# Kernel tuning notes

Measured on AMD Instinct MI355X. Metric: run time of the kernel, lower is better.

Reference implementation:

```python
import jax, jax.numpy as jnp
import numpy as np

EPS_NORM = 1e-12  # F.normalize eps
LN_EPS = 1e-5


def _ln(x, g, b):
    mu = x.mean(-1, keepdims=True)
    var = ((x - mu) ** 2).mean(-1, keepdims=True)
    return (x - mu) / jnp.sqrt(var + LN_EPS) * g + b


def _gate(x, w1, b1, g, b, w2, b2):
    # Linear -> LayerNorm(32) -> SiLU -> Linear -> Sigmoid, squeeze(-1)
    t = _ln(x @ w1 + b1, g, b)
    t = jax.nn.silu(t)
    return jax.nn.sigmoid(t @ w2 + b2)[..., 0]


def setup_inputs() -> dict:
    key = jax.random.key(0)
    B, N, D, dH, S, HID = 4, 4096, 1024, 256, 256, 32
    ks = jax.random.split(key, 24)
    sc_d = 0.5 * (6.0 / (D + dH)) ** 0.5  # xavier gain=0.5 approx
    sc_h = 0.5 * (6.0 / (D + HID)) ** 0.5
    inp = {
        "h": jax.random.normal(ks[0], (B, N, D), jnp.float32),
        # encoder complex projection (stored as (in,out))
        "Wr": jax.random.uniform(ks[1], (D, dH), jnp.float32, -sc_d, sc_d),
        "br": jnp.zeros((dH,), jnp.float32),
        "Wi": jax.random.uniform(ks[2], (D, dH), jnp.float32, -sc_d, sc_d),
        "bi": jnp.zeros((dH,), jnp.float32),
        # uncertainty net
        "uw1": jax.random.uniform(ks[3], (D, HID), jnp.float32, -sc_h, sc_h),
        "ub1": jnp.zeros((HID,), jnp.float32),
        "ug": jnp.ones((HID,), jnp.float32),
        "ubeta": jnp.zeros((HID,), jnp.float32),
        "uw2": jax.random.uniform(ks[4], (HID, 1), jnp.float32, -0.2, 0.2),
        "ub2": jnp.zeros((1,), jnp.float32),
        # decoherence gamma net
        "gw1": jax.random.uniform(ks[5], (D, HID), jnp.float32, -sc_h, sc_h),
        "gb1": jnp.zeros((HID,), jnp.float32),
        "gg": jnp.ones((HID,), jnp.float32),
        "gbeta": jnp.zeros((HID,), jnp.float32),
        "gw2": jax.random.uniform(ks[6], (HID, 1), jnp.float32, -0.2, 0.2),
        "gb2": jnp.zeros((1,), jnp.float32),
        # memory attention params
        "m_real": jax.random.normal(ks[7], (S, dH), jnp.float32) / dH ** 0.5,
        "m_imag": jax.random.normal(ks[8], (S, dH), jnp.float32) / dH ** 0.5,
        "values": jax.random.normal(ks[9], (S, D), jnp.float32) * 0.02,
        "ow": jax.random.uniform(ks[10], (D, D), jnp.float32, -0.5 * (3.0 / D) ** 0.5, 0.5 * (3.0 / D) ** 0.5),
        "ob": jnp.zeros((D,), jnp.float32),
        # norms
        "n1g": jnp.ones((D,), jnp.float32),
        "n1b": jnp.zeros((D,), jnp.float32),
        "n2g": jnp.ones((D,), jnp.float32),
        "n2b": jnp.zeros((D,), jnp.float32),
        # FFN
        "fw1": jax.random.normal(ks[11], (D, 4 * D), jnp.float32) * (2.0 / (5 * D)) ** 0.5,
        "fb1": jnp.zeros((4 * D,), jnp.float32),
        "fw2": jax.random.normal(ks[12], (4 * D, D), jnp.float32) * (2.0 / (5 * D)) ** 0.5,
        "fb2": jnp.zeros((D,), jnp.float32),
    }
    return inp


def reference(h, Wr, br, Wi, bi,
              uw1, ub1, ug, ubeta, uw2, ub2,
              gw1, gb1, gg, gbeta, gw2, gb2,
              m_real, m_imag, values, ow, ob,
              n1g, n1b, n2g, n2b, fw1, fb1, fw2, fb2):
    dH = m_real.shape[-1]
    # --- QuantumStateEncoder: psi = normalize(complex(Wr h, Wi h)), p in [0,0.95]
    pr = h @ Wr + br                       # (B,N,dH) real part
    pi = h @ Wi + bi                       # (B,N,dH) imag part
    nrm = jnp.maximum(jnp.sqrt(jnp.sum(pr * pr + pi * pi, -1, keepdims=True)), EPS_NORM)
    pr, pi = pr / nrm, pi / nrm
    p_init = _gate(h, uw1, ub1, ug, ubeta, uw2, ub2) * 0.95   # (B,N)
    # --- ContextualDecoherenceLayer: ctx = mean over N (identical per token)
    ctx = h.mean(axis=1)                   # (B,D)
    gamma = _gate(ctx, gw1, gb1, gg, gbeta, gw2, gb2)          # (B,)
    p = p_init * (1.0 - gamma[:, None])    # (B,N)
    # --- ExternalQuantumMemoryAttention
    mnrm = jnp.maximum(jnp.sqrt(jnp.sum(m_real * m_real + m_imag * m_imag, -1, keepdims=True)), EPS_NORM)
    Mr, Mi = m_real / mnrm, m_imag / mnrm  # (S,dH)
    # <psi|m> = sum conj(psi)*m ; |.|^2 is re^2+im^2
    re = jnp.einsum('bnd,sd->bns', pr, Mr) + jnp.einsum('bnd,sd->bns', pi, Mi)
    im = jnp.einsum('bnd,sd->bns', pr, Mi) - jnp.einsum('bnd,sd->bns', pi, Mr)
    overlap = re * re + im * im            # (B,N,S)
    raw = (1.0 - p)[..., None] * overlap + (p / dH)[..., None]
    attn = raw / (raw.sum(-1, keepdims=True) + 1e-8)
    attn_out = jnp.einsum('bns,sd->bnd', attn, values) @ ow + ob
    # --- residual + LN + FFN (dropout = eval identity)
    h1 = _ln(h + attn_out, n1g, n1b)
    ff = jax.nn.gelu(h1 @ fw1 + fb1, approximate=False) @ fw2 + fb2
    return _ln(h1 + ff, n2g, n2b)
```

## Files before the change

### kernel.cpp

```cpp
#include <hip/hip_runtime.h>
#include <math.h>


#define B_ 4
#define N_ 4096
#define D_ 1024
#define DH_ 256
#define S_ 256
#define HID_ 32
#define M_ (B_ * N_)

typedef unsigned short u16;
typedef unsigned int u32;
typedef __attribute__((ext_vector_type(8))) short bfrag;
typedef __attribute__((ext_vector_type(4))) float ffrag;

__device__ __forceinline__ float b2f(u16 u) {
    return __uint_as_float(((unsigned)u) << 16);
}
__device__ __forceinline__ u16 f2b(float f) {
    unsigned u = __float_as_uint(f);
    return (u16)((u + 0x7FFFu + ((u >> 16) & 1u)) >> 16);
}
__device__ __forceinline__ float fast_erf(float x) {
    float ax = fabsf(x);
    float t = __builtin_amdgcn_rcpf(fmaf(0.3275911f, ax, 1.f));
    float p = t * fmaf(t, fmaf(t, fmaf(t, fmaf(t, 1.061405429f, -1.453152027f),
                                       1.421413741f), -0.284496736f),
                       0.254829592f);
    float e = __expf(-ax * ax);
    float y = fmaf(-p, e, 1.f);
    return copysignf(y, x);
}
__device__ __forceinline__ float gelu_fast(float x) {
    return 0.5f * x * (1.0f + fast_erf(x * 0.70710678118654752440f));
}
__device__ __forceinline__ float ldf(const void* p, size_t i, bool bf) {
    return bf ? b2f(((const u16*)p)[i]) : ((const float*)p)[i];
}
__device__ __forceinline__ bool detect_bf(const void* n1g) {
    return *(const unsigned*)n1g == 0x3F803F80u;
}
__device__ __forceinline__ void gload16(const void* g, void* lds) {
    __builtin_amdgcn_global_load_lds(
        (const __attribute__((address_space(1))) u32*)g,
        (__attribute__((address_space(3))) u32*)lds, 16, 0, 0);
}

__global__ void zero_kernel(float* __restrict__ p, int n) {
    int i = blockIdx.x * 256 + threadIdx.x;
    if (i < n) p[i] = 0.f;
}

__global__ __launch_bounds__(256)
void h2b_kernel(const void* __restrict__ h, u16* __restrict__ hB,
                const void* __restrict__ n1g) {
    const bool bf = detect_bf(n1g);
    const size_t i = ((size_t)blockIdx.x * 256 + threadIdx.x) * 8;
    if (bf) {
        *(uint4*)(hB + i) = *(const uint4*)((const u16*)h + i);
    } else {
        const float* hf = (const float*)h;
        float4 x = *(const float4*)(hf + i);
        float4 y = *(const float4*)(hf + i + 4);
        union { u16 u[8]; uint4 v; } pk;
        pk.u[0] = f2b(x.x); pk.u[1] = f2b(x.y);
        pk.u[2] = f2b(x.z); pk.u[3] = f2b(x.w);
        pk.u[4] = f2b(y.x); pk.u[5] = f2b(y.y);
        pk.u[6] = f2b(y.z); pk.u[7] = f2b(y.w);
        *(uint4*)(hB + i) = pk.v;
    }
}

__global__ void pack_bias_kernel(const void* __restrict__ br,
                                 const void* __restrict__ bi,
                                 void* __restrict__ brbi,
                                 const void* __restrict__ n1g) {
    const bool bf = detect_bf(n1g);
    const int t = threadIdx.x;
    if (bf) {
        ((u16*)brbi)[t]       = ((const u16*)br)[t];
        ((u16*)brbi)[256 + t] = ((const u16*)bi)[t];
    } else {
        ((float*)brbi)[t]       = ((const float*)br)[t];
        ((float*)brbi)[256 + t] = ((const float*)bi)[t];
    }
}

__global__ __launch_bounds__(256)
void transpose_w_kernel(const void* __restrict__ W, u16* __restrict__ WT,
                        int K, int N, const void* __restrict__ n1g) {
    const bool bf = detect_bf(n1g);
    __shared__ u16 t[64][65];
    const int n0 = blockIdx.x * 64, k0 = blockIdx.y * 64;
    const int a = threadIdx.x & 63, b = threadIdx.x >> 6;
#pragma unroll
    for (int r = 0; r < 16; ++r) {
        int k = b * 16 + r;
        t[k][a] = f2b(ldf(W, (size_t)(k0 + k) * N + n0 + a, bf));
    }
    __syncthreads();
#pragma unroll
    for (int r = 0; r < 16; ++r) {
        int n = b * 16 + r;
        WT[(size_t)(n0 + n) * K + k0 + a] = t[a][n];
    }
}

__global__ __launch_bounds__(256)
void ctx_sum_kernel(const u16* __restrict__ hB, float* __restrict__ ctx) {
    const int chunks = N_ / 128;
    const int b = blockIdx.x / chunks;
    const int ch = blockIdx.x % chunks;
    const int tid = threadIdx.x;
    const size_t base = ((size_t)b * N_ + (size_t)ch * 128) * D_;
    float a[4] = {0.f, 0.f, 0.f, 0.f};
    for (int r = 0; r < 128; ++r)
#pragma unroll
        for (int q = 0; q < 4; ++q)
            a[q] += b2f(hB[base + (size_t)r * D_ + q * 256 + tid]);
#pragma unroll
    for (int q = 0; q < 4; ++q)
        atomicAdd(&ctx[b * D_ + q * 256 + tid], a[q]);
}

__global__ __launch_bounds__(128)
void gamma_gate_kernel(const float* __restrict__ ctx,
                       const void* __restrict__ w1, const void* __restrict__ b1,
                       const void* __restrict__ g, const void* __restrict__ beta,
                       const void* __restrict__ w2, const void* __restrict__ b2,
                       float* __restrict__ out, const void* __restrict__ n1g) {
    const bool bf = detect_bf(n1g);
    const int row = blockIdx.x;
    const int tid = threadIdx.x;
    const int col = tid & 31;
    const int chunk = tid >> 5;
    const float xscale = 1.f / (float)N_;

    float acc = 0.f;
    for (int k = chunk * 256; k < chunk * 256 + 256; ++k)
        acc += ctx[(size_t)row * D_ + k] * xscale * ldf(w1, (size_t)k * HID_ + col, bf);

    __shared__ float part[4][HID_];
    __shared__ float s[HID_];
    __shared__ float mu_s, rstd_s;
    part[chunk][col] = acc;
    __syncthreads();
    if (tid < HID_)
        s[tid] = part[0][tid] + part[1][tid] + part[2][tid] + part[3][tid]
               + ldf(b1, tid, bf);
    __syncthreads();
    if (tid == 0) {
        float m = 0.f;
        for (int i = 0; i < HID_; ++i) m += s[i];
        m /= (float)HID_;
        float var = 0.f;
        for (int i = 0; i < HID_; ++i) { float dd = s[i] - m; var += dd * dd; }
        var /= (float)HID_;
        mu_s = m;
        rstd_s = rsqrtf(var + 1e-5f);
    }
    __syncthreads();
    if (tid < HID_) {
        float v = (s[tid] - mu_s) * rstd_s * ldf(g, tid, bf) + ldf(beta, tid, bf);
        v = v / (1.f + expf(-v));
        s[tid] = v * ldf(w2, tid, bf);
    }
    __syncthreads();
    if (tid == 0) {
        float z = 0.f;
        for (int i = 0; i < HID_; ++i) z += s[i];
        z += ldf(b2, 0, bf);
        out[row] = 1.f / (1.f + expf(-z));
    }
}

__global__ __launch_bounds__(128)
void p_gate_kernel(const u16* __restrict__ hB,
                   const void* __restrict__ w1, const void* __restrict__ b1,
                   const void* __restrict__ g, const void* __restrict__ beta,
                   const void* __restrict__ w2, const void* __restrict__ b2,
                   float* __restrict__ out, const void* __restrict__ n1g) {
    const bool bf = detect_bf(n1g);
    const int row = blockIdx.x;
    const int tid = threadIdx.x;
    const int col = tid & 31;
    const int chunk = tid >> 5;

    float acc = 0.f;
    for (int k = chunk * 256; k < chunk * 256 + 256; ++k)
        acc += b2f(hB[(size_t)row * D_ + k]) * ldf(w1, (size_t)k * HID_ + col, bf);

    __shared__ float part[4][HID_];
    __shared__ float s[HID_];
    __shared__ float mu_s, rstd_s;
    part[chunk][col] = acc;
    __syncthreads();
    if (tid < HID_)
        s[tid] = part[0][tid] + part[1][tid] + part[2][tid] + part[3][tid]
               + ldf(b1, tid, bf);
    __syncthreads();
    if (tid == 0) {
        float m = 0.f;
        for (int i = 0; i < HID_; ++i) m += s[i];
        m /= (float)HID_;
        float var = 0.f;
        for (int i = 0; i < HID_; ++i) { float dd = s[i] - m; var += dd * dd; }
        var /= (float)HID_;
        mu_s = m;
        rstd_s = rsqrtf(var + 1e-5f);
    }
    __syncthreads();
    if (tid < HID_) {
        float v = (s[tid] - mu_s) * rstd_s * ldf(g, tid, bf) + ldf(beta, tid, bf);
        v = v / (1.f + expf(-v));
        s[tid] = v * ldf(w2, tid, bf);
    }
    __syncthreads();
    if (tid == 0) {
        float z = 0.f;
        for (int i = 0; i < HID_; ++i) z += s[i];
        z += ldf(b2, 0, bf);
        out[row] = 0.95f / (1.f + expf(-z));
    }
}

__global__ __launch_bounds__(256)
void norm_m_kernel(const void* __restrict__ m_real, const void* __restrict__ m_imag,
                   u16* __restrict__ bcatT, const void* __restrict__ n1g) {
    const bool bf = detect_bf(n1g);
    const int s = blockIdx.x;
    const int d = threadIdx.x;
    float mr = ldf(m_real, (size_t)s * DH_ + d, bf);
    float mi = ldf(m_imag, (size_t)s * DH_ + d, bf);
    float v = mr * mr + mi * mi;
#pragma unroll
    for (int off = 32; off; off >>= 1) v += __shfl_down(v, off, 64);
    __shared__ float red[4];
    if ((d & 63) == 0) red[d >> 6] = v;
    __syncthreads();
    float tot = red[0] + red[1] + red[2] + red[3];
    float inv = 1.f / fmaxf(sqrtf(tot), 1e-12f);
    float nr = mr * inv, ni = mi * inv;
    bcatT[(size_t)s * 512 + d]               = f2b(nr);
    bcatT[(size_t)s * 512 + 256 + d]         = f2b(ni);
    bcatT[(size_t)(256 + s) * 512 + d]       = f2b(ni);
    bcatT[(size_t)(256 + s) * 512 + 256 + d] = f2b(-nr);
}

__global__ __launch_bounds__(256)
void gemm_mfma(const u16* __restrict__ A, const u16* __restrict__ WT,
               const void* __restrict__ bias, void* __restrict__ out,
               int N, int kseg, int lda, int ldw, int ldo,
               int act, int fo32, int accum, const void* __restrict__ n1g) {
    const bool bf = detect_bf(n1g);
    __shared__ short As[128 * 64];
    __shared__ short Bs[128 * 64];
    const int tid = threadIdx.x;

    const int nwg = gridDim.x * gridDim.y;
    const int flat = blockIdx.y * gridDim.x + blockIdx.x;
    const int xcd = flat & 7, idx = flat >> 3;
    const int qq = nwg >> 3, rr = nwg & 7;
    const int nf = (xcd < rr ? xcd * (qq + 1) : rr * (qq + 1) + (xcd - rr) * qq) + idx;
    const int c0 = (nf % gridDim.x) * 128;
    const int r0 = (nf / gridDim.x) * 128;

    const int kz = blockIdx.z * kseg;
    const int lane = tid & 63, wave = tid >> 6;
    const int wm = wave & 1, wn = wave >> 1;
    const int quad = lane >> 4, l15 = lane & 15;
    const int l8 = lane >> 3;
    const int lc = (lane & 7) ^ l8;
    const int sx = l15 & 7;

    ffrag acc[4][4];
#pragma unroll
    for (int i = 0; i < 4; ++i)
#pragma unroll
        for (int j = 0; j < 4; ++j)
            acc[i][j] = (ffrag){0.f, 0.f, 0.f, 0.f};

    for (int k0 = kz; k0 < kz + kseg; k0 += 64) {
        __syncthreads();
#pragma unroll
        for (int i = 0; i < 4; ++i) {
            int rb = wave * 32 + i * 8;
            gload16(A + (size_t)(r0 + rb + l8) * lda + k0 + lc * 8,
                    &As[rb * 64]);
        }
#pragma unroll
        for (int i = 0; i < 4; ++i) {
            int rb = wave * 32 + i * 8;
            gload16(WT + (size_t)(c0 + rb + l8) * ldw + k0 + lc * 8,
                    &Bs[rb * 64]);
        }
        __syncthreads();

#pragma unroll
        for (int ks = 0; ks < 2; ++ks) {
            bfrag a[4], b[4];
#pragma unroll
            for (int i = 0; i < 4; ++i) {
                int row = wm * 64 + i * 16 + l15;
                a[i] = *(const bfrag*)&As[row * 64 + (((ks * 4 + quad) ^ sx) * 8)];
            }
#pragma unroll
            for (int j = 0; j < 4; ++j) {
                int row = wn * 64 + j * 16 + l15;
                b[j] = *(const bfrag*)&Bs[row * 64 + (((ks * 4 + quad) ^ sx) * 8)];
            }
#pragma unroll
            for (int i = 0; i < 4; ++i)
#pragma unroll
                for (int j = 0; j < 4; ++j)
                    acc[i][j] = __builtin_amdgcn_mfma_f32_16x16x32_bf16(
                        a[i], b[j], acc[i][j], 0, 0, 0);
        }
    }

    const bool addb = bias && (blockIdx.z == 0);
    float bv[4];
#pragma unroll
    for (int j = 0; j < 4; ++j)
        bv[j] = addb ? ldf(bias, c0 + wn * 64 + j * 16 + l15, bf) : 0.f;
#pragma unroll
    for (int i = 0; i < 4; ++i)
#pragma unroll
        for (int r = 0; r < 4; ++r) {
            int row_g = r0 + wm * 64 + i * 16 + quad * 4 + r;
#pragma unroll
            for (int j = 0; j < 4; ++j) {
                int col_g = c0 + wn * 64 + j * 16 + l15;
                float v = acc[i][j][r] + bv[j];
                if (act) v = gelu_fast(v);
                if (accum)
                    atomicAdd(&((float*)out)[(size_t)row_g * ldo + col_g], v);
                else if (fo32)
                    ((float*)out)[(size_t)row_g * ldo + col_g] = v;
                else
                    ((u16*)out)[(size_t)row_g * ldo + col_g] = f2b(v);
            }
        }
}

#define TPW 8
__global__ __launch_bounds__(256)
void attn_weights_kernel(const u16* __restrict__ psi,
                         const float* __restrict__ reim,
                         const float* __restrict__ p_init,
                         const float* __restrict__ gamma,
                         u16* __restrict__ a2) {
    const int token0 = blockIdx.x * TPW;
    const int tid = threadIdx.x;
    __shared__ float red[4];

    for (int tt = 0; tt < TPW; ++tt) {
        const size_t t = (size_t)(token0 + tt);
        float x0 = b2f(psi[t * 512 + tid]);
        float x1 = b2f(psi[t * 512 + 256 + tid]);
        float v = x0 * x0 + x1 * x1;
#pragma unroll
        for (int off = 32; off; off >>= 1) v += __shfl_down(v, off, 64);
        if ((tid & 63) == 0) red[tid >> 6] = v;
        __syncthreads();
        float inv = 1.f / fmaxf(red[0] + red[1] + red[2] + red[3], 1e-24f);

        float p = p_init[t] * (1.f - gamma[t / N_]);
        float re = reim[t * 512 + tid];
        float im = reim[t * 512 + 256 + tid];
        float raw = (1.f - p) * (re * re + im * im) * inv + p * (1.f / (float)DH_);

        float w = raw;
#pragma unroll
        for (int off = 32; off; off >>= 1) w += __shfl_down(w, off, 64);
        __syncthreads();
        if ((tid & 63) == 0) red[tid >> 6] = w;
        __syncthreads();
        float denom = red[0] + red[1] + red[2] + red[3];
        a2[t * 256 + tid] = f2b(raw / (denom + 1e-8f));
        __syncthreads();
    }
}

__global__ __launch_bounds__(256)
void copy_rows_kernel(const u16* __restrict__ src, u16* __restrict__ dst) {
    const int row = blockIdx.x;
    const int tid = threadIdx.x;
#pragma unroll
    for (int q = 0; q < 4; ++q)
        dst[(size_t)row * D_ + q * 256 + tid] = src[(size_t)row * D_ + q * 256 + tid];
}

__global__ __launch_bounds__(256)
void ln_add_kernel(const void* __restrict__ x, int xmode, size_t xrow0,
                   const void* __restrict__ y, int ymode,
                   const void* __restrict__ g, const void* __restrict__ b,
                   u16* __restrict__ outB, float* __restrict__ outF,
                   const void* __restrict__ n1g) {
    const bool bfin = detect_bf(n1g);
    const bool bfx = (xmode == 1) ? true : bfin;
    const int row = blockIdx.x;
    const int tid = threadIdx.x;
    __shared__ float red[4];

    float v[4];
#pragma unroll
    for (int q = 0; q < 4; ++q) {
        int d = q * 256 + tid;
        float yv = ymode ? ((const float*)y)[(size_t)row * D_ + d]
                         : b2f(((const u16*)y)[(size_t)row * D_ + d]);
        v[q] = ldf(x, (xrow0 + row) * (size_t)D_ + d, bfx) + yv;
    }

    float s = v[0] + v[1] + v[2] + v[3];
#pragma unroll
    for (int off = 32; off; off >>= 1) s += __shfl_down(s, off, 64);
    if ((tid & 63) == 0) red[tid >> 6] = s;
    __syncthreads();
    float mu = (red[0] + red[1] + red[2] + red[3]) * (1.f / (float)D_);
    __syncthreads();

    float q2 = 0.f;
#pragma unroll
    for (int j = 0; j < 4; ++j) { float dd = v[j] - mu; q2 += dd * dd; }
#pragma unroll
    for (int off = 32; off; off >>= 1) q2 += __shfl_down(q2, off, 64);
    if ((tid & 63) == 0) red[tid >> 6] = q2;
    __syncthreads();
    float var = (red[0] + red[1] + red[2] + red[3]) * (1.f / (float)D_);
    float rstd = rsqrtf(var + 1e-5f);

#pragma unroll
    for (int q = 0; q < 4; ++q) {
        int d = q * 256 + tid;
        float o = (v[q] - mu) * rstd * ldf(g, d, bfin) + ldf(b, d, bfin);
        if (outF) outF[(size_t)row * D_ + d] = o;
        else      outB[(size_t)row * D_ + d] = f2b(o);
    }
}

extern "C" void kernel_launch(void* const* d_in, const int* in_sizes, int n_in,
                              void* d_out, int out_size, void* d_ws, size_t ws_size,
                              hipStream_t stream) {
    const void* h      = d_in[0];
    const void* Wr     = d_in[1];
    const void* br     = d_in[2];
    const void* Wi     = d_in[3];
    const void* bi     = d_in[4];
    const void* uw1    = d_in[5];
    const void* ub1    = d_in[6];
    const void* ug     = d_in[7];
    const void* ubeta  = d_in[8];
    const void* uw2    = d_in[9];
    const void* ub2    = d_in[10];
    const void* gw1    = d_in[11];
    const void* gb1    = d_in[12];
    const void* gg     = d_in[13];
    const void* gbeta  = d_in[14];
    const void* gw2    = d_in[15];
    const void* gb2    = d_in[16];
    const void* m_real = d_in[17];
    const void* m_imag = d_in[18];
    const void* values = d_in[19];
    const void* ow     = d_in[20];
    const void* ob     = d_in[21];
    const void* n1g    = d_in[22];
    const void* n1b    = d_in[23];
    const void* n2g    = d_in[24];
    const void* n2b    = d_in[25];
    const void* fw1    = d_in[26];
    const void* fb1    = d_in[27];
    const void* fw2    = d_in[28];
    const void* fb2    = d_in[29];

    char*  ws      = (char*)d_ws;
    float* ctx     = (float*)(ws);
    float* gammap  = (float*)(ws + 16384);
    float* p_init  = (float*)(ws + 16448);
    void*  brbi    = (void*)(ws + 81984);
    u16*   BCatT   = (u16*)(ws + 84032);
    u16*   WrT     = (u16*)(ws + 608320);
    u16*   WiT     = (u16*)(ws + 1132608);
    u16*   valuesT = (u16*)(ws + 1656896);
    u16*   owT     = (u16*)(ws + 2181184);
    u16*   fw1T    = (u16*)(ws + 4278336);
    u16*   fw2T    = (u16*)(ws + 12666944);
    const size_t tbase = 21055552;

    int CH = 16384;
    while (CH > 128 && tbase + (size_t)CH * 12288 > ws_size) CH >>= 1;
    u16*   t_buf = (u16*)(ws + tbase);
    float* pf    = (float*)(t_buf + (size_t)CH * 4096);

    float* outF   = (float*)d_out;
    u16*   Psi    = (u16*)d_out;
    u16*   A2     = Psi + (size_t)M_ * 512;
    u16*   X2     = (u16*)d_out + (size_t)M_ * D_;
    u16*   hB     = X2;
    float* REIMf  = (float*)X2;

    h2b_kernel<<<M_ * D_ / 2048, 256, 0, stream>>>(h, hB, n1g);

    transpose_w_kernel<<<dim3(DH_ / 64, D_ / 64), 256, 0, stream>>>(Wr, WrT, D_, DH_, n1g);
    transpose_w_kernel<<<dim3(DH_ / 64, D_ / 64), 256, 0, stream>>>(Wi, WiT, D_, DH_, n1g);
    transpose_w_kernel<<<dim3(D_ / 64, S_ / 64), 256, 0, stream>>>(values, valuesT, S_, D_, n1g);
    transpose_w_kernel<<<dim3(D_ / 64, D_ / 64), 256, 0, stream>>>(ow, owT, D_, D_, n1g);
    transpose_w_kernel<<<dim3(4 * D_ / 64, D_ / 64), 256, 0, stream>>>(fw1, fw1T, D_, 4 * D_, n1g);
    transpose_w_kernel<<<dim3(D_ / 64, 4 * D_ / 64), 256, 0, stream>>>(fw2, fw2T, 4 * D_, D_, n1g);
    pack_bias_kernel<<<1, 256, 0, stream>>>(br, bi, brbi, n1g);

    zero_kernel<<<16, 256, 0, stream>>>(ctx, B_ * D_);
    ctx_sum_kernel<<<B_ * (N_ / 128), 256, 0, stream>>>(hB, ctx);
    gamma_gate_kernel<<<B_, 128, 0, stream>>>(ctx, gw1, gb1, gg, gbeta,
                                              gw2, gb2, gammap, n1g);

    norm_m_kernel<<<S_, 256, 0, stream>>>(m_real, m_imag, BCatT, n1g);

    gemm_mfma<<<dim3(512 / 128, M_ / 128), 256, 0, stream>>>(
        hB, WrT, brbi, Psi, 512, D_, D_, D_, 512, 0, 0, 0, n1g);

    p_gate_kernel<<<M_, 128, 0, stream>>>(hB, uw1, ub1, ug, ubeta,
                                          uw2, ub2, p_init, n1g);

    gemm_mfma<<<dim3(512 / 128, M_ / 128), 256, 0, stream>>>(
        Psi, BCatT, nullptr, REIMf, 512, 512, 512, 512, 512, 0, 1, 0, n1g);

    attn_weights_kernel<<<M_ / TPW, 256, 0, stream>>>(Psi, REIMf, p_init,
                                                      gammap, A2);

    gemm_mfma<<<dim3(D_ / 128, M_ / 128), 256, 0, stream>>>(
        A2, valuesT, nullptr, X2, D_, S_, S_, S_, D_, 0, 0, 0, n1g);

    const int gy = CH / 128;
    auto pick_split = [&](int gx) {
        int ks = 1;
        while (gx * gy * ks < 512 && ks < 8) ks <<= 1;
        return ks;
    };

    {
        const int ks = pick_split(D_ / 128);
        for (int c = 0; c < M_ / CH; ++c) {
            const size_t off = (size_t)c * CH * D_;
            if (ks > 1)
                zero_kernel<<<(CH * D_ + 255) / 256, 256, 0, stream>>>(pf, CH * D_);
            gemm_mfma<<<dim3(D_ / 128, gy, ks), 256, 0, stream>>>(
                X2 + off, owT, ob, pf, D_, D_ / ks, D_, D_, D_, 0, 1, ks > 1, n1g);
            ln_add_kernel<<<CH, 256, 0, stream>>>(h, 0, (size_t)c * CH, pf, 1,
                                                  n1g, n1b, X2 + off, nullptr, n1g);
        }
    }

    {
        const int ks2 = pick_split(D_ / 128);
        for (int c = 0; c < M_ / CH; ++c) {
            const size_t off = (size_t)c * CH * D_;
            gemm_mfma<<<dim3(4 * D_ / 128, gy), 256, 0, stream>>>(
                X2 + off, fw1T, fb1, t_buf, 4 * D_, D_, D_, D_, 4 * D_, 1, 0, 0, n1g);
            if (ks2 > 1)
                zero_kernel<<<(CH * D_ + 255) / 256, 256, 0, stream>>>(pf, CH * D_);
            gemm_mfma<<<dim3(D_ / 128, gy, ks2), 256, 0, stream>>>(
                t_buf, fw2T, fb2, pf, D_, 4 * D_ / ks2, 4 * D_, 4 * D_, D_, 0, 1, ks2 > 1, n1g);
            copy_rows_kernel<<<CH, 256, 0, stream>>>(X2 + off, t_buf);
            ln_add_kernel<<<CH, 256, 0, stream>>>(t_buf, 1, 0, pf, 1,
                                                  n2g, n2b, nullptr, outF + off, n1g);
        }
    }
}
```

Before: 1.068 ms.

## Add 256x256 double-buffered MFMA GEMM and drop split-K atomics for large GEMMs

Adds a new 512-thread GEMM kernel with 256x256 output tiles, double-buffered LDS staging overlapped via vmcnt waits, and raised wave priority during the MFMA phase. It is used for the values, output-projection and both FFN GEMMs. The split-K path with atomicAdd and its zeroing kernels is removed. Larger tiles raise data reuse and cut global traffic. The cost is higher register and LDS use (128 KB LDS per block), which lowers occupancy, and fewer workgroups when the chunk size is small.

Result: faster. 1.013 ms (-5.2%).

```diff
diff --git a/kernel.cpp b/kernel.cpp
--- a/kernel.cpp
+++ b/kernel.cpp
@@ -251,8 +251,8 @@
 __global__ __launch_bounds__(256)
 void gemm_mfma(const u16* __restrict__ A, const u16* __restrict__ WT,
                const void* __restrict__ bias, void* __restrict__ out,
-               int N, int kseg, int lda, int ldw, int ldo,
-               int act, int fo32, int accum, const void* __restrict__ n1g) {
+               int kseg, int lda, int ldw, int ldo,
+               int act, int fo32, const void* __restrict__ n1g) {
     const bool bf = detect_bf(n1g);
     __shared__ short As[128 * 64];
     __shared__ short Bs[128 * 64];
@@ -266,7 +266,6 @@
     const int c0 = (nf % gridDim.x) * 128;
     const int r0 = (nf / gridDim.x) * 128;
 
-    const int kz = blockIdx.z * kseg;
     const int lane = tid & 63, wave = tid >> 6;
     const int wm = wave & 1, wn = wave >> 1;
     const int quad = lane >> 4, l15 = lane & 15;
@@ -281,19 +280,17 @@
         for (int j = 0; j < 4; ++j)
             acc[i][j] = (ffrag){0.f, 0.f, 0.f, 0.f};
 
-    for (int k0 = kz; k0 < kz + kseg; k0 += 64) {
+    for (int k0 = 0; k0 < kseg; k0 += 64) {
         __syncthreads();
 #pragma unroll
         for (int i = 0; i < 4; ++i) {
             int rb = wave * 32 + i * 8;
-            gload16(A + (size_t)(r0 + rb + l8) * lda + k0 + lc * 8,
-                    &As[rb * 64]);
+            gload16(A + (size_t)(r0 + rb + l8) * lda + k0 + lc * 8, &As[rb * 64]);
         }
 #pragma unroll
         for (int i = 0; i < 4; ++i) {
             int rb = wave * 32 + i * 8;
-            gload16(WT + (size_t)(c0 + rb + l8) * ldw + k0 + lc * 8,
-                    &Bs[rb * 64]);
+            gload16(WT + (size_t)(c0 + rb + l8) * ldw + k0 + lc * 8, &Bs[rb * 64]);
         }
         __syncthreads();
 
@@ -319,11 +316,10 @@
         }
     }
 
-    const bool addb = bias && (blockIdx.z == 0);
     float bv[4];
 #pragma unroll
     for (int j = 0; j < 4; ++j)
-        bv[j] = addb ? ldf(bias, c0 + wn * 64 + j * 16 + l15, bf) : 0.f;
+        bv[j] = bias ? ldf(bias, c0 + wn * 64 + j * 16 + l15, bf) : 0.f;
 #pragma unroll
     for (int i = 0; i < 4; ++i)
 #pragma unroll
@@ -334,12 +330,112 @@
                 int col_g = c0 + wn * 64 + j * 16 + l15;
                 float v = acc[i][j][r] + bv[j];
                 if (act) v = gelu_fast(v);
-                if (accum)
-                    atomicAdd(&((float*)out)[(size_t)row_g * ldo + col_g], v);
-                else if (fo32)
-                    ((float*)out)[(size_t)row_g * ldo + col_g] = v;
-                else
-                    ((u16*)out)[(size_t)row_g * ldo + col_g] = f2b(v);
+                if (fo32) ((float*)out)[(size_t)row_g * ldo + col_g] = v;
+                else      ((u16*)out)[(size_t)row_g * ldo + col_g] = f2b(v);
+            }
+        }
+}
+
+__global__ __launch_bounds__(512, 2)
+void gemm_mfma2(const u16* __restrict__ A, const u16* __restrict__ WT,
+                const void* __restrict__ bias, void* __restrict__ out,
+                int K, int lda, int ldw, int ldo,
+                int act, int fo32, const void* __restrict__ n1g) {
+    const bool bf = detect_bf(n1g);
+    __shared__ short As[2][256 * 64];
+    __shared__ short Bs[2][256 * 64];
+    const int tid = threadIdx.x;
+
+    const int nwg = gridDim.x * gridDim.y;
+    const int flat = blockIdx.y * gridDim.x + blockIdx.x;
+    const int xcd = flat & 7, idx = flat >> 3;
+    const int qq = nwg >> 3, rr = nwg & 7;
+    const int nf = (xcd < rr ? xcd * (qq + 1) : rr * (qq + 1) + (xcd - rr) * qq) + idx;
+    const int c0 = (nf % gridDim.x) * 256;
+    const int r0 = (nf / gridDim.x) * 256;
+
+    const int lane = tid & 63, wave = tid >> 6;
+    const int wm = wave & 1, wn = wave >> 1;
+    const int quad = lane >> 4, l15 = lane & 15;
+    const int l8 = lane >> 3;
+    const int lc = (lane & 7) ^ l8;
+    const int sx = l15 & 7;
+
+    ffrag acc[8][4];
+#pragma unroll
+    for (int i = 0; i < 8; ++i)
+#pragma unroll
+        for (int j = 0; j < 4; ++j)
+            acc[i][j] = (ffrag){0.f, 0.f, 0.f, 0.f};
+
+    auto STAGE = [&](int buf, int k0) {
+#pragma unroll
+        for (int r = 0; r < 4; ++r) {
+            int rb = r * 64 + wave * 8;
+            gload16(A + (size_t)(r0 + rb + l8) * lda + k0 + lc * 8,
+                    &As[buf][rb * 64]);
+        }
+#pragma unroll
+        for (int r = 0; r < 4; ++r) {
+            int rb = r * 64 + wave * 8;
+            gload16(WT + (size_t)(c0 + rb + l8) * ldw + k0 + lc * 8,
+                    &Bs[buf][rb * 64]);
+        }
+    };
+
+    const int nt = K >> 6;
+    STAGE(0, 0);
+    int cur = 0;
+    for (int t = 0; t < nt; ++t) {
+        if (t + 1 < nt) {
+            STAGE(cur ^ 1, (t + 1) << 6);
+            asm volatile("s_waitcnt vmcnt(8)" ::: "memory");
+        } else {
+            asm volatile("s_waitcnt vmcnt(0)" ::: "memory");
+        }
+        __builtin_amdgcn_s_barrier();
+        __builtin_amdgcn_sched_barrier(0);
+        __builtin_amdgcn_s_setprio(1);
+#pragma unroll
+        for (int ks = 0; ks < 2; ++ks) {
+            bfrag a[8], b[4];
+#pragma unroll
+            for (int j = 0; j < 4; ++j) {
+                int row = wn * 64 + j * 16 + l15;
+                b[j] = *(const bfrag*)&Bs[cur][row * 64 + (((ks * 4 + quad) ^ sx) * 8)];
+            }
+#pragma unroll
+            for (int i = 0; i < 8; ++i) {
+                int row = wm * 128 + i * 16 + l15;
+                a[i] = *(const bfrag*)&As[cur][row * 64 + (((ks * 4 + quad) ^ sx) * 8)];
+#pragma unroll
+                for (int j = 0; j < 4; ++j)
+                    acc[i][j] = __builtin_amdgcn_mfma_f32_16x16x32_bf16(
+                        a[i], b[j], acc[i][j], 0, 0, 0);
+            }
+        }
+        __builtin_amdgcn_s_setprio(0);
+        __builtin_amdgcn_sched_barrier(0);
+        __builtin_amdgcn_s_barrier();
+        cur ^= 1;
+    }
+
+    float bv[4];
+#pragma unroll
+    for (int j = 0; j < 4; ++j)
+        bv[j] = bias ? ldf(bias, c0 + wn * 64 + j * 16 + l15, bf) : 0.f;
+#pragma unroll
+    for (int i = 0; i < 8; ++i)
+#pragma unroll
+        for (int r = 0; r < 4; ++r) {
+            int row_g = r0 + wm * 128 + i * 16 + quad * 4 + r;
+#pragma unroll
+            for (int j = 0; j < 4; ++j) {
+                int col_g = c0 + wn * 64 + j * 16 + l15;
+                float v = acc[i][j][r] + bv[j];
+                if (act) v = gelu_fast(v);
+                if (fo32) ((float*)out)[(size_t)row_g * ldo + col_g] = v;
+                else      ((u16*)out)[(size_t)row_g * ldo + col_g] = f2b(v);
             }
         }
 }
@@ -489,7 +585,7 @@
     const size_t tbase = 21055552;
 
     int CH = 16384;
-    while (CH > 128 && tbase + (size_t)CH * 12288 > ws_size) CH >>= 1;
+    while (CH > 256 && tbase + (size_t)CH * 12288 > ws_size) CH >>= 1;
     u16*   t_buf = (u16*)(ws + tbase);
     float* pf    = (float*)(t_buf + (size_t)CH * 4096);
 
@@ -518,53 +614,36 @@
     norm_m_kernel<<<S_, 256, 0, stream>>>(m_real, m_imag, BCatT, n1g);
 
     gemm_mfma<<<dim3(512 / 128, M_ / 128), 256, 0, stream>>>(
-        hB, WrT, brbi, Psi, 512, D_, D_, D_, 512, 0, 0, 0, n1g);
+        hB, WrT, brbi, Psi, D_, D_, D_, 512, 0, 0, n1g);
 
     p_gate_kernel<<<M_, 128, 0, stream>>>(hB, uw1, ub1, ug, ubeta,
                                           uw2, ub2, p_init, n1g);
 
     gemm_mfma<<<dim3(512 / 128, M_ / 128), 256, 0, stream>>>(
-        Psi, BCatT, nullptr, REIMf, 512, 512, 512, 512, 512, 0, 1, 0, n1g);
+        Psi, BCatT, nullptr, REIMf, 512, 512, 512, 512, 0, 1, n1g);
 
     attn_weights_kernel<<<M_ / TPW, 256, 0, stream>>>(Psi, REIMf, p_init,
                                                       gammap, A2);
 
-    gemm_mfma<<<dim3(D_ / 128, M_ / 128), 256, 0, stream>>>(
-        A2, valuesT, nullptr, X2, D_, S_, S_, S_, D_, 0, 0, 0, n1g);
-
-    const int gy = CH / 128;
-    auto pick_split = [&](int gx) {
-        int ks = 1;
-        while (gx * gy * ks < 512 && ks < 8) ks <<= 1;
-        return ks;
-    };
-
-    {
-        const int ks = pick_split(D_ / 128);
-        for (int c = 0; c < M_ / CH; ++c) {
-            const size_t off = (size_t)c * CH * D_;
-            if (ks > 1)
-                zero_kernel<<<(CH * D_ + 255) / 256, 256, 0, stream>>>(pf, CH * D_);
-            gemm_mfma<<<dim3(D_ / 128, gy, ks), 256, 0, stream>>>(
-                X2 + off, owT, ob, pf, D_, D_ / ks, D_, D_, D_, 0, 1, ks > 1, n1g);
-            ln_add_kernel<<<CH, 256, 0, stream>>>(h, 0, (size_t)c * CH, pf, 1,
-                                                  n1g, n1b, X2 + off, nullptr, n1g);
-        }
-    }
-
-    {
-        const int ks2 = pick_split(D_ / 128);
-        for (int c = 0; c < M_ / CH; ++c) {
-            const size_t off = (size_t)c * CH * D_;
-            gemm_mfma<<<dim3(4 * D_ / 128, gy), 256, 0, stream>>>(
-                X2 + off, fw1T, fb1, t_buf, 4 * D_, D_, D_, D_, 4 * D_, 1, 0, 0, n1g);
-            if (ks2 > 1)
-                zero_kernel<<<(CH * D_ + 255) / 256, 256, 0, stream>>>(pf, CH * D_);
-            gemm_mfma<<<dim3(D_ / 128, gy, ks2), 256, 0, stream>>>(
-                t_buf, fw2T, fb2, pf, D_, 4 * D_ / ks2, 4 * D_, 4 * D_, D_, 0, 1, ks2 > 1, n1g);
-            copy_rows_kernel<<<CH, 256, 0, stream>>>(X2 + off, t_buf);
-            ln_add_kernel<<<CH, 256, 0, stream>>>(t_buf, 1, 0, pf, 1,
-                                                  n2g, n2b, nullptr, outF + off, n1g);
-        }
-    }
-}
+    gemm_mfma2<<<dim3(D_ / 256, M_ / 256), 512, 0, stream>>>(
+        A2, valuesT, nullptr, X2, S_, S_, S_, D_, 0, 0, n1g);
+
+    for (int c = 0; c < M_ / CH; ++c) {
+        const size_t off = (size_t)c * CH * D_;
+        gemm_mfma2<<<dim3(D_ / 256, CH / 256), 512, 0, stream>>>(
+            X2 + off, owT, ob, pf, D_, D_, D_, D_, 0, 1, n1g);
+        ln_add_kernel<<<CH, 256, 0, stream>>>(h, 0, (size_t)c * CH, pf, 1,
+                                              n1g, n1b, X2 + off, nullptr, n1g);
+    }
+
+    for (int c = 0; c < M_ / CH; ++c) {
+        const size_t off = (size_t)c * CH * D_;
+        gemm_mfma2<<<dim3(4 * D_ / 256, CH / 256), 512, 0, stream>>>(
+            X2 + off, fw1T, fb1, t_buf, D_, D_, D_, 4 * D_, 1, 0, n1g);
+        gemm_mfma2<<<dim3(D_ / 256, CH / 256), 512, 0, stream>>>(
+            t_buf, fw2T, fb2, pf, 4 * D_, 4 * D_, 4 * D_, D_, 0, 1, n1g);
+        copy_rows_kernel<<<CH, 256, 0, stream>>>(X2 + off, t_buf);
+        ln_add_kernel<<<CH, 256, 0, stream>>>(t_buf, 1, 0, pf, 1,
+                                              n2g, n2b, nullptr, outF + off, n1g);
+    }
+}
```
